# Optimization experiments

Hardware: AMD Instinct MI355X
Metric: run time of the kernel (lower is better)

The kernel has to match this reference:

```python
import jax, jax.numpy as jnp
import numpy as np


def setup_inputs() -> dict:
    key = jax.random.key(0)
    k1, = jax.random.split(key, 1)
    N, H, C, T = 4, 16, 64, 2048
    qkv = jax.random.normal(k1, (N, 3 * H * C, T), dtype=jnp.float32)
    mask = jnp.ones((N, T), dtype=jnp.float32)
    return {"qkv": qkv, "mask": mask, "n_heads": H}


def reference(qkv, mask, n_heads):
    bs, width, length = qkv.shape
    ch = width // (3 * n_heads)
    # [bs*H, 3*ch, T] -> split into q, k, v each [bs*H, ch, T]
    qkv_r = qkv.reshape(bs * n_heads, ch * 3, length)
    q, k, v = qkv_r[:, :ch], qkv_r[:, ch:2 * ch], qkv_r[:, 2 * ch:]
    scale = 1.0 / (ch ** 0.25)  # scale applied to both q and k, as in original
    weight = jnp.einsum('bct,bcs->bts', q * scale, k * scale)  # [bs*H, T, T]
    weight = jax.nn.softmax(weight.astype(jnp.float32), axis=-1).astype(qkv.dtype)
    # torch mask.repeat(n_heads, 1).unsqueeze(1) == tile over leading dim -> [bs*H, 1, T]
    mask_r = jnp.tile(mask, (n_heads, 1))[:, None, :]
    weight = weight * mask_r  # post-softmax multiply (faithful to original)
    a = jnp.einsum('bts,bcs->bct', weight, v)  # [bs*H, ch, T]
    return a.reshape(bs, -1, length)
```

## Files before the change

kernel.cpp:

```cpp
#include <hip/hip_runtime.h>

typedef __attribute__((ext_vector_type(4))) float f32x4;
typedef __attribute__((ext_vector_type(8))) short s16x8;
typedef __attribute__((ext_vector_type(4))) short s16x4;

constexpr int T_SEQ = 2048;
constexpr int D = 64;
constexpr int H = 16;
constexpr int QBLK = 128;
constexpr int KVBLK = 64;
constexpr int NTHREADS = 512;

__device__ __forceinline__ unsigned short f2bf(float f) {
  unsigned int u = __builtin_bit_cast(unsigned int, f);
  u += 0x7FFFu + ((u >> 16) & 1u);
  return (unsigned short)(u >> 16);
}

__device__ __forceinline__ int swz(int row, int colByte) {
  return row * 128 + (colByte ^ ((row & 7) << 4));
}

__global__ __launch_bounds__(NTHREADS, 4)
void attn_kernel(const float* __restrict__ qkv, const float* __restrict__ mask,
                 float* __restrict__ out) {
  __shared__ __align__(16) char smem[33024];
  char* Qc = smem;
  char* Kc = smem;
  char* Vc = smem + 8192;
  char* Pc = smem + 16384;
  float* maskS = (float*)(smem + 32768);

  const int tid = threadIdx.x;
  const int qt = blockIdx.x;
  const int bh = blockIdx.y;
  const int b = bh >> 4, h = bh & 15;

  const size_t headBase = ((size_t)b * (3 * H * D) + (size_t)h * (3 * D)) * T_SEQ;
  const float* gQ = qkv + headBase;
  const float* gK = gQ + (size_t)D * T_SEQ;
  const float* gV = gQ + (size_t)(2 * D) * T_SEQ;
  const float* gM = mask + (size_t)(bh & 3) * T_SEQ;

  {
    const int sb = (tid & 31) * 4;
    const int cb = (tid >> 5) * 4;
    const int q0 = qt * QBLK;
    f32x4 r[4];
#pragma unroll
    for (int j = 0; j < 4; ++j)
      r[j] = *(const f32x4*)(gQ + (size_t)(cb + j) * T_SEQ + q0 + sb);
#pragma unroll
    for (int i = 0; i < 4; ++i) {
      s16x4 w;
#pragma unroll
      for (int j = 0; j < 4; ++j) w[j] = (short)f2bf(r[j][i] * 0.125f);
      *(s16x4*)(Qc + swz(sb + i, 2 * cb)) = w;
    }
  }
  __syncthreads();

  const int wave = tid >> 6, lane = tid & 63;
  const int lg = lane >> 4, lid = lane & 15;

  s16x8 aq[2];
#pragma unroll
  for (int ko = 0; ko < 2; ++ko)
    aq[ko] = *(const s16x8*)(Qc + swz(wave * 16 + lid, 16 * lg + 64 * ko));

  float m0 = -1e30f, l0 = 0.0f;
  f32x4 accO[4];
#pragma unroll
  for (int ct = 0; ct < 4; ++ct) accO[ct] = (f32x4){0.f, 0.f, 0.f, 0.f};

  char* Pw = Pc + wave * 2048;

  for (int s0 = 0; s0 < T_SEQ; s0 += KVBLK) {
    __syncthreads();
    if (tid < 256) {
      const int sb = (tid & 15) * 4;
      const int cb = (tid >> 4) * 4;
      f32x4 r[4];
#pragma unroll
      for (int j = 0; j < 4; ++j)
        r[j] = *(const f32x4*)(gK + (size_t)(cb + j) * T_SEQ + s0 + sb);
#pragma unroll
      for (int i = 0; i < 4; ++i) {
        s16x4 w;
#pragma unroll
        for (int j = 0; j < 4; ++j) w[j] = (short)f2bf(r[j][i]);
        *(s16x4*)(Kc + swz(sb + i, 2 * cb)) = w;
      }
    } else {
      const int t = tid - 256;
      const int c = t >> 2;
      const int sbase = (t & 3) * 16;
      f32x4 r[4];
#pragma unroll
      for (int j = 0; j < 4; ++j)
        r[j] = *(const f32x4*)(gV + (size_t)c * T_SEQ + s0 + sbase + 4 * j);
      s16x8 w0, w1;
#pragma unroll
      for (int j = 0; j < 8; ++j) w0[j] = (short)f2bf(r[j >> 2][j & 3]);
#pragma unroll
      for (int j = 0; j < 8; ++j) w1[j] = (short)f2bf(r[2 + (j >> 2)][j & 3]);
      *(s16x8*)(Vc + swz(c, 2 * sbase)) = w0;
      *(s16x8*)(Vc + swz(c, 2 * sbase + 16)) = w1;
      if (tid >= 448) maskS[tid - 448] = gM[s0 + tid - 448];
    }
    __syncthreads();

    f32x4 accST[4];
#pragma unroll
    for (int nt = 0; nt < 4; ++nt) accST[nt] = (f32x4){0.f, 0.f, 0.f, 0.f};
#pragma unroll
    for (int ko = 0; ko < 2; ++ko) {
#pragma unroll
      for (int nt = 0; nt < 4; ++nt) {
        s16x8 ak = *(const s16x8*)(Kc + swz(nt * 16 + lid, 16 * lg + 64 * ko));
        accST[nt] = __builtin_amdgcn_mfma_f32_16x16x32_bf16(ak, aq[ko], accST[nt], 0, 0, 0);
      }
    }

    float tm = accST[0][0];
#pragma unroll
    for (int nt = 0; nt < 4; ++nt) {
#pragma unroll
      for (int r = 0; r < 4; ++r) tm = fmaxf(tm, accST[nt][r]);
    }
    tm = fmaxf(tm, __shfl_xor(tm, 16));
    tm = fmaxf(tm, __shfl_xor(tm, 32));
    if (!__all(tm - m0 <= 8.0f)) {
      const float nm = fmaxf(m0, tm);
      const float sc = __expf(m0 - nm);
      m0 = nm;
      l0 *= sc;
#pragma unroll
      for (int ct = 0; ct < 4; ++ct) {
#pragma unroll
        for (int r = 0; r < 4; ++r) accO[ct][r] *= sc;
      }
    }
    float p[4][4], rs = 0.0f;
#pragma unroll
    for (int nt = 0; nt < 4; ++nt) {
#pragma unroll
      for (int r = 0; r < 4; ++r) {
        p[nt][r] = __expf(accST[nt][r] - m0);
        rs += p[nt][r];
      }
    }
    rs += __shfl_xor(rs, 16);
    rs += __shfl_xor(rs, 32);
    l0 += rs;

#pragma unroll
    for (int nt = 0; nt < 4; ++nt) {
      const f32x4 mk = *(const f32x4*)&maskS[16 * nt + 4 * lg];
      s16x4 w;
#pragma unroll
      for (int r = 0; r < 4; ++r) w[r] = (short)f2bf(p[nt][r] * mk[r]);
      *(s16x4*)(Pw + swz(lid, 32 * nt + 8 * lg)) = w;
    }

#pragma unroll
    for (int ko = 0; ko < 2; ++ko) {
      s16x8 bp = *(const s16x8*)(Pw + swz(lid, 64 * ko + 16 * lg));
#pragma unroll
      for (int ct = 0; ct < 4; ++ct) {
        s16x8 av = *(const s16x8*)(Vc + swz(ct * 16 + lid, 64 * ko + 16 * lg));
        accO[ct] = __builtin_amdgcn_mfma_f32_16x16x32_bf16(av, bp, accO[ct], 0, 0, 0);
      }
    }
  }

  const float rcp = 1.0f / l0;
  const int qcol = qt * QBLK + wave * 16 + lid;
#pragma unroll
  for (int ct = 0; ct < 4; ++ct) {
#pragma unroll
    for (int r = 0; r < 4; ++r) {
      const int c = 16 * ct + 4 * lg + r;
      out[((size_t)(b * (H * D) + h * D + c)) * T_SEQ + qcol] = accO[ct][r] * rcp;
    }
  }
}

extern "C" void kernel_launch(void* const* d_in, const int* in_sizes, int n_in,
                              void* d_out, int out_size, void* d_ws, size_t ws_size,
                              hipStream_t stream) {
  const float* qkv = (const float*)d_in[0];
  const float* mask = (const float*)d_in[1];
  float* out = (float*)d_out;
  dim3 grid(T_SEQ / QBLK, 64);
  attn_kernel<<<grid, NTHREADS, 0, stream>>>(qkv, mask, out);
}
```

Baseline: 313.6 us.

## Fold mask into V, use exp2 softmax, swizzle block order, add MFMA priority

```diff
diff --git a/kernel.cpp b/kernel.cpp
--- a/kernel.cpp
+++ b/kernel.cpp
@@ -1,6 +1,8 @@
 #include <hip/hip_runtime.h>
+#include <hip/hip_bf16.h>
 
 typedef __attribute__((ext_vector_type(4))) float f32x4;
+typedef __attribute__((ext_vector_type(2))) float f32x2;
 typedef __attribute__((ext_vector_type(8))) short s16x8;
 typedef __attribute__((ext_vector_type(4))) short s16x4;
 
@@ -10,30 +12,39 @@
 constexpr int QBLK = 128;
 constexpr int KVBLK = 64;
 constexpr int NTHREADS = 512;
-
-__device__ __forceinline__ unsigned short f2bf(float f) {
-  unsigned int u = __builtin_bit_cast(unsigned int, f);
-  u += 0x7FFFu + ((u >> 16) & 1u);
-  return (unsigned short)(u >> 16);
+constexpr float LOG2E = 1.44269504088896340736f;
+
+__device__ __forceinline__ short f2bf(float f) {
+  return (short)__builtin_bit_cast(unsigned short, __float2bfloat16(f));
+}
+
+__device__ __forceinline__ float fast_exp2(float x) {
+#if __has_builtin(__builtin_amdgcn_exp2f)
+  return __builtin_amdgcn_exp2f(x);
+#else
+  return exp2f(x);
+#endif
 }
 
 __device__ __forceinline__ int swz(int row, int colByte) {
   return row * 128 + (colByte ^ ((row & 7) << 4));
 }
 
-__global__ __launch_bounds__(NTHREADS, 4)
+__global__ __launch_bounds__(NTHREADS, 6)
 void attn_kernel(const float* __restrict__ qkv, const float* __restrict__ mask,
                  float* __restrict__ out) {
-  __shared__ __align__(16) char smem[33024];
+  __shared__ __align__(16) char smem[40960];
   char* Qc = smem;
   char* Kc = smem;
   char* Vc = smem + 8192;
   char* Pc = smem + 16384;
-  float* maskS = (float*)(smem + 32768);
+  float* maskLds = (float*)(smem + 32768);
 
   const int tid = threadIdx.x;
-  const int qt = blockIdx.x;
-  const int bh = blockIdx.y;
+  int flat = blockIdx.y * 16 + blockIdx.x;
+  flat = (flat & 7) * 128 + (flat >> 3);
+  const int qt = flat & 15;
+  const int bh = flat >> 4;
   const int b = bh >> 4, h = bh & 15;
 
   const size_t headBase = ((size_t)b * (3 * H * D) + (size_t)h * (3 * D)) * T_SEQ;
@@ -42,10 +53,12 @@
   const float* gV = gQ + (size_t)(2 * D) * T_SEQ;
   const float* gM = mask + (size_t)(bh & 3) * T_SEQ;
 
+  *(f32x4*)&maskLds[tid * 4] = *(const f32x4*)&gM[tid * 4];
   {
     const int sb = (tid & 31) * 4;
     const int cb = (tid >> 5) * 4;
     const int q0 = qt * QBLK;
+    const float qscale = 0.125f * LOG2E;
     f32x4 r[4];
 #pragma unroll
     for (int j = 0; j < 4; ++j)
@@ -54,7 +67,7 @@
     for (int i = 0; i < 4; ++i) {
       s16x4 w;
 #pragma unroll
-      for (int j = 0; j < 4; ++j) w[j] = (short)f2bf(r[j][i] * 0.125f);
+      for (int j = 0; j < 4; ++j) w[j] = f2bf(r[j][i] * qscale);
       *(s16x4*)(Qc + swz(sb + i, 2 * cb)) = w;
     }
   }
@@ -78,41 +91,44 @@
   for (int s0 = 0; s0 < T_SEQ; s0 += KVBLK) {
     __syncthreads();
     if (tid < 256) {
-      const int sb = (tid & 15) * 4;
-      const int cb = (tid >> 4) * 4;
-      f32x4 r[4];
-#pragma unroll
-      for (int j = 0; j < 4; ++j)
-        r[j] = *(const f32x4*)(gK + (size_t)(cb + j) * T_SEQ + s0 + sb);
-#pragma unroll
-      for (int i = 0; i < 4; ++i) {
-        s16x4 w;
-#pragma unroll
-        for (int j = 0; j < 4; ++j) w[j] = (short)f2bf(r[j][i]);
-        *(s16x4*)(Kc + swz(sb + i, 2 * cb)) = w;
+      const int sb = 2 * (tid & 31);
+      const int cb = 8 * (tid >> 5);
+      f32x2 r[8];
+#pragma unroll
+      for (int j = 0; j < 8; ++j)
+        r[j] = *(const f32x2*)(gK + (size_t)(cb + j) * T_SEQ + s0 + sb);
+#pragma unroll
+      for (int i = 0; i < 2; ++i) {
+        s16x8 w;
+#pragma unroll
+        for (int j = 0; j < 8; ++j) w[j] = f2bf(r[j][i]);
+        *(s16x8*)(Kc + swz(sb + i, 2 * cb)) = w;
       }
     } else {
-      const int t = tid - 256;
-      const int c = t >> 2;
-      const int sbase = (t & 3) * 16;
-      f32x4 r[4];
-#pragma unroll
-      for (int j = 0; j < 4; ++j)
+      const int t2 = tid - 256;
+      const int c = t2 >> 2;
+      const int sbase = 16 * (t2 & 3);
+      f32x4 r[4], mk[4];
+#pragma unroll
+      for (int j = 0; j < 4; ++j) {
         r[j] = *(const f32x4*)(gV + (size_t)c * T_SEQ + s0 + sbase + 4 * j);
+        mk[j] = *(const f32x4*)&maskLds[s0 + sbase + 4 * j];
+      }
       s16x8 w0, w1;
 #pragma unroll
-      for (int j = 0; j < 8; ++j) w0[j] = (short)f2bf(r[j >> 2][j & 3]);
-#pragma unroll
-      for (int j = 0; j < 8; ++j) w1[j] = (short)f2bf(r[2 + (j >> 2)][j & 3]);
+      for (int j = 0; j < 8; ++j) w0[j] = f2bf(r[j >> 2][j & 3] * mk[j >> 2][j & 3]);
+#pragma unroll
+      for (int j = 0; j < 8; ++j)
+        w1[j] = f2bf(r[2 + (j >> 2)][j & 3] * mk[2 + (j >> 2)][j & 3]);
       *(s16x8*)(Vc + swz(c, 2 * sbase)) = w0;
       *(s16x8*)(Vc + swz(c, 2 * sbase + 16)) = w1;
-      if (tid >= 448) maskS[tid - 448] = gM[s0 + tid - 448];
     }
     __syncthreads();
 
     f32x4 accST[4];
 #pragma unroll
     for (int nt = 0; nt < 4; ++nt) accST[nt] = (f32x4){0.f, 0.f, 0.f, 0.f};
+    __builtin_amdgcn_s_setprio(1);
 #pragma unroll
     for (int ko = 0; ko < 2; ++ko) {
 #pragma unroll
@@ -121,18 +137,19 @@
         accST[nt] = __builtin_amdgcn_mfma_f32_16x16x32_bf16(ak, aq[ko], accST[nt], 0, 0, 0);
       }
     }
-
-    float tm = accST[0][0];
-#pragma unroll
-    for (int nt = 0; nt < 4; ++nt) {
-#pragma unroll
-      for (int r = 0; r < 4; ++r) tm = fmaxf(tm, accST[nt][r]);
-    }
+    __builtin_amdgcn_s_setprio(0);
+
+    float mx[4];
+#pragma unroll
+    for (int nt = 0; nt < 4; ++nt)
+      mx[nt] = fmaxf(fmaxf(accST[nt][0], accST[nt][1]),
+                     fmaxf(accST[nt][2], accST[nt][3]));
+    float tm = fmaxf(fmaxf(mx[0], mx[1]), fmaxf(mx[2], mx[3]));
     tm = fmaxf(tm, __shfl_xor(tm, 16));
     tm = fmaxf(tm, __shfl_xor(tm, 32));
-    if (!__all(tm - m0 <= 8.0f)) {
+    if (!__all(tm - m0 <= 11.5416f)) {
       const float nm = fmaxf(m0, tm);
-      const float sc = __expf(m0 - nm);
+      const float sc = fast_exp2(m0 - nm);
       m0 = nm;
       l0 *= sc;
 #pragma unroll
@@ -141,28 +158,27 @@
         for (int r = 0; r < 4; ++r) accO[ct][r] *= sc;
       }
     }
-    float p[4][4], rs = 0.0f;
+    float p[4][4], ps[4];
 #pragma unroll
     for (int nt = 0; nt < 4; ++nt) {
 #pragma unroll
-      for (int r = 0; r < 4; ++r) {
-        p[nt][r] = __expf(accST[nt][r] - m0);
-        rs += p[nt][r];
-      }
-    }
+      for (int r = 0; r < 4; ++r) p[nt][r] = fast_exp2(accST[nt][r] - m0);
+      ps[nt] = (p[nt][0] + p[nt][1]) + (p[nt][2] + p[nt][3]);
+    }
+    float rs = (ps[0] + ps[1]) + (ps[2] + ps[3]);
     rs += __shfl_xor(rs, 16);
     rs += __shfl_xor(rs, 32);
     l0 += rs;
 
 #pragma unroll
     for (int nt = 0; nt < 4; ++nt) {
-      const f32x4 mk = *(const f32x4*)&maskS[16 * nt + 4 * lg];
       s16x4 w;
 #pragma unroll
-      for (int r = 0; r < 4; ++r) w[r] = (short)f2bf(p[nt][r] * mk[r]);
+      for (int r = 0; r < 4; ++r) w[r] = f2bf(p[nt][r]);
       *(s16x4*)(Pw + swz(lid, 32 * nt + 8 * lg)) = w;
     }
 
+    __builtin_amdgcn_s_setprio(1);
 #pragma unroll
     for (int ko = 0; ko < 2; ++ko) {
       s16x8 bp = *(const s16x8*)(Pw + swz(lid, 64 * ko + 16 * lg));
@@ -172,6 +188,7 @@
         accO[ct] = __builtin_amdgcn_mfma_f32_16x16x32_bf16(av, bp, accO[ct], 0, 0, 0);
       }
     }
+    __builtin_amdgcn_s_setprio(0);
   }
 
   const float rcp = 1.0f / l0;
```

Result: faster. 277.1 us (-11.6%).
